# Kernel tuning notes

Measured on AMD Instinct MI355X. Metric: run time of the kernel, lower is better.

The kernel has to match this reference:

```python
import jax, jax.numpy as jnp
import numpy as np

N_NODES = 50000
N_EDGES = 800000
N_FEAT = 64
N_HID = 64
N_CLASSES = 10
N_GRAPHS = 64


def setup_inputs() -> dict:
    key = jax.random.key(0)
    ks = jax.random.split(key, 14)
    # edge_index with no self-loops (PyG add_remaining_self_loops then appends
    # exactly one self loop per node, which the reference reproduces)
    row = jax.random.randint(ks[0], (N_EDGES,), 0, N_NODES, dtype=jnp.int32)
    off = jax.random.randint(ks[1], (N_EDGES,), 1, N_NODES, dtype=jnp.int32)
    col = (row + off) % N_NODES
    edge_index = jnp.stack([row, col])
    batch = jnp.sort(jax.random.randint(ks[2], (N_NODES,), 0, N_GRAPHS, dtype=jnp.int32))
    x = jax.random.normal(ks[3], (N_NODES, N_FEAT), jnp.float32)
    P_vec = jax.random.normal(ks[4], (N_EDGES,), jnp.float32)

    def lin(k, fi, fo):
        return jax.random.normal(k, (fi, fo), jnp.float32) * (1.0 / np.sqrt(fi))

    return {
        "x": x, "edge_index": edge_index, "batch": batch, "P_vec": P_vec,
        "W1": lin(ks[5], N_FEAT, N_HID), "b1": jax.random.normal(ks[6], (N_HID,)) * 0.02,
        "W2": lin(ks[7], N_HID, N_HID), "b2": jax.random.normal(ks[8], (N_HID,)) * 0.02,
        "W3": lin(ks[9], N_HID, N_HID), "b3": jax.random.normal(ks[10], (N_HID,)) * 0.02,
        "Wl": lin(ks[11], N_HID, N_CLASSES), "bl": jax.random.normal(ks[12], (N_CLASSES,)) * 0.02,
    }


def reference(x, edge_index, batch, P_vec, W1, b1, W2, b2, W3, b3, Wl, bl):
    n = x.shape[0]
    row, col = edge_index[0], edge_index[1]
    # add_remaining_self_loops: append one self loop per node with weight 1.0
    sl = jnp.arange(n, dtype=row.dtype)
    fr = jnp.concatenate([row, sl])          # [E+N] source
    fc = jnp.concatenate([col, sl])          # [E+N] target (flow source_to_target)
    w = jnp.concatenate([jax.nn.sigmoid(P_vec), jnp.ones((n,), x.dtype)])
    deg = jax.ops.segment_sum(w, fc, num_segments=n)
    dis = jnp.where(deg > 0, deg ** -0.5, 0.0)  # deg_inv_sqrt, inf->0
    norm = dis[fr] * w * dis[fc]             # identical for all 3 conv layers

    def gcn_layer(h, W, b):
        h = h @ W                             # Linear (no bias inside lin)
        agg = jax.ops.segment_sum(norm[:, None] * h[fr], fc, num_segments=n)
        return agg + b

    h = jax.nn.relu(gcn_layer(x, W1, b1))
    h = jax.nn.relu(gcn_layer(h, W2, b2))
    h = gcn_layer(h, W3, b3)
    # global_mean_pool over batch segment ids
    sums = jax.ops.segment_sum(h, batch, num_segments=N_GRAPHS)
    cnt = jax.ops.segment_sum(jnp.ones((n, 1), h.dtype), batch, num_segments=N_GRAPHS)
    pooled = sums / jnp.maximum(cnt, 1.0)
    # dropout is identity at inference; final classifier
    return pooled @ Wl + bl
```

## Files before the change

### kernel.cpp

```cpp
#include <hip/hip_runtime.h>
#include <hip/hip_bf16.h>
#include <hip/hip_fp16.h>
#include <math.h>

#define N_GRAPHS 64
#define N_CLASSES 10
#define FIXSCALE 262144.0f
#define MAXDEG 64

typedef __hip_bfloat16 bf16;
typedef int          i32x4 __attribute__((ext_vector_type(4)));
typedef unsigned int u32x4 __attribute__((ext_vector_type(4)));
typedef _Float16     f16x8 __attribute__((ext_vector_type(8)));
typedef float        f32x4 __attribute__((ext_vector_type(4)));

__device__ __forceinline__ unsigned int pack_edge(int r, float s) {
    return ((unsigned int)r << 16) | (unsigned int)__half_as_ushort(__float2half(s));
}

__global__ void init_k(const float* __restrict__ P, const int* __restrict__ row,
                       unsigned int* __restrict__ packed, uint2* __restrict__ pre,
                       float* __restrict__ sums, float* __restrict__ cntG,
                       int n, int E) {
    int i = blockIdx.x * 256 + threadIdx.x;
    if (i < n) packed[i] = 0u;
    if (i < N_GRAPHS * 64) sums[i] = 0.0f;
    if (i < N_GRAPHS) cntG[i] = 0.0f;
    if (i < E) {
        float s = 1.0f / (1.0f + expf(-P[i]));
        pre[i] = make_uint2(pack_edge(row[i], s), (unsigned int)(s * FIXSCALE + 0.5f));
    }
}

__device__ __forceinline__ int bucket_of(int c) {
    int b = (int)(((unsigned int)c * 41u) >> 18);
    return b > 7 ? 7 : b;
}

__device__ __forceinline__ void do_edge(int c, unsigned int rec, unsigned int fix, int myb,
                                        unsigned int* __restrict__ packed,
                                        unsigned int* __restrict__ ell) {
    if (bucket_of(c) == myb) {
        unsigned int old = atomicAdd(&packed[c], (1u << 24) | fix);
        unsigned int rank = old >> 24;
        if (rank < MAXDEG) ell[c * MAXDEG + rank] = rec;
    }
}

__global__ __launch_bounds__(256) void hist_k(const uint2* __restrict__ pre,
                                              const int* __restrict__ col,
                                              unsigned int* __restrict__ packed,
                                              unsigned int* __restrict__ ell, int E) {
    const int myb = blockIdx.x & 7;
    const int slice = blockIdx.x >> 3;
    const int E4 = E >> 2;
    const i32x4* col4 = (const i32x4*)col;
    const u32x4* pre4 = (const u32x4*)pre;
#pragma unroll
    for (int k = 0; k < 4; ++k) {
        int i4 = slice * 1024 + k * 256 + (int)threadIdx.x;
        if (i4 < E4) {
            i32x4 c  = col4[i4];
            u32x4 pa = pre4[2 * i4];
            u32x4 pb = pre4[2 * i4 + 1];
            do_edge(c[0], pa[0], pa[1], myb, packed, ell);
            do_edge(c[1], pa[2], pa[3], myb, packed, ell);
            do_edge(c[2], pb[0], pb[1], myb, packed, ell);
            do_edge(c[3], pb[2], pb[3], myb, packed, ell);
        }
    }
    if (slice == 0) {
        for (int e = E4 * 4 + (int)threadIdx.x; e < E; e += 256) {
            uint2 p = pre[e];
            do_edge(col[e], p.x, p.y, myb, packed, ell);
        }
    }
}

__global__ void disxg_k(const unsigned int* __restrict__ packed,
                        const float* __restrict__ x,
                        float* __restrict__ dis, bf16* __restrict__ xg,
                        unsigned int* __restrict__ ell, int n) {
    int i = blockIdx.x * 256 + threadIdx.x;
    if (i < n * 64) {
        int node = i >> 6;
        int lane = i & 63;
        unsigned int pk = packed[node];
        float deg = 1.0f + (float)(pk & 0xFFFFFFu) * (1.0f / FIXSCALE);
        float dv = 1.0f / sqrtf(deg);
        xg[i] = __float2bfloat16(x[i] * dv);
        if (lane == 0) dis[node] = dv;
        int cnt = (int)(pk >> 24);
        if (cnt > MAXDEG) cnt = MAXDEG;
        int pad = ((cnt + 15) & ~15) - cnt;
        if (lane < pad) ell[node * MAXDEG + cnt + lane] = 0u;
    }
}

__global__ void fold_k(const float* __restrict__ W3, const float* __restrict__ b3,
                       const float* __restrict__ Wl, const float* __restrict__ bl,
                       const float* __restrict__ W1, const float* __restrict__ W2,
                       float* __restrict__ Wc, float* __restrict__ bc,
                       __half* __restrict__ W1h, __half* __restrict__ W2h) {
    int t = blockIdx.x * 256 + threadIdx.x;
    if (t < 64 * N_CLASSES) {
        int k = t / N_CLASSES, c = t % N_CLASSES;
        float acc = 0.0f;
        for (int m = 0; m < 64; ++m) acc += W3[k * 64 + m] * Wl[m * N_CLASSES + c];
        Wc[t] = acc;
    }
    if (t < N_CLASSES) {
        float acc = bl[t];
        for (int m = 0; m < 64; ++m) acc += b3[m] * Wl[m * N_CLASSES + t];
        bc[t] = acc;
    }
    if (t < 8192) {
        int u = t & 4095;
        int j = u & 7, lane = (u >> 3) & 63, k2 = (u >> 9) & 1, tt = u >> 10;
        int srow = k2 * 32 + (lane >> 4) * 8 + j;
        int scol = tt * 16 + (lane & 15);
        const float* W = (t < 4096) ? W1 : W2;
        __half* Wh = (t < 4096) ? W1h : W2h;
        Wh[u] = __float2half(W[srow * 64 + scol]);
    }
}

__device__ __forceinline__ float edge_term(unsigned int v, const bf16* g, int lane) {
    int r = (int)(v >> 16);
    float s = __half2float(__ushort_as_half((unsigned short)(v & 0xFFFFu)));
    return s * __bfloat162float(g[r * 64 + lane]);
}

template <int OUTF>
__global__ __launch_bounds__(256) void agg_k(const bf16* __restrict__ g,
                                             const unsigned int* __restrict__ ell,
                                             const unsigned int* __restrict__ packed,
                                             const float* __restrict__ dis,
                                             float* __restrict__ out,
                                             __half* __restrict__ outH, int n) {
    int tid = threadIdx.x;
    int node = __builtin_amdgcn_readfirstlane(blockIdx.x * 4 + (tid >> 6));
    if (node >= n) return;
    int lane = tid & 63;

    float d = dis[node];
    int cnt = (int)(packed[node] >> 24);
    if (cnt > MAXDEG) cnt = MAXDEG;
    int cnt16 = (cnt + 15) & ~15;
    float acc = __bfloat162float(g[node * 64 + lane]);
    const unsigned int* rowp = ell + node * MAXDEG;

    float a[16];
#pragma unroll
    for (int t = 0; t < 16; ++t) a[t] = 0.0f;
    for (int j = 0; j < cnt16; j += 16) {
        unsigned int v[16];
#pragma unroll
        for (int t = 0; t < 16; ++t) v[t] = rowp[j + t];
#pragma unroll
        for (int t = 0; t < 16; ++t) a[t] += edge_term(v[t], g, lane);
    }
#pragma unroll
    for (int off = 8; off >= 1; off >>= 1)
#pragma unroll
        for (int t = 0; t < off; ++t) a[t] += a[t + off];
    acc += a[0];
    acc *= d;

    if (OUTF == 1) outH[(size_t)node * 64 + lane] = __float2half(acc);
    else           out[(size_t)node * 64 + lane] = acc;
}

__global__ __launch_bounds__(256) void gemm_k(const __half* __restrict__ A,
                                              const __half* __restrict__ Wsw,
                                              const float* __restrict__ b,
                                              const float* __restrict__ dis,
                                              bf16* __restrict__ outg, int n) {
    int tid = threadIdx.x;
    int grp = blockIdx.x * 4 + (tid >> 6);
    int rbase = grp * 16;
    if (rbase >= n) return;
    int l = tid & 63, lr = l & 15, lh = l >> 4;

    const f16x8* Ap = (const f16x8*)(A + (size_t)(rbase + lr) * 64 + lh * 8);
    f16x8 a0 = Ap[0];
    f16x8 a1 = Ap[4];
    const f16x8* Wp = (const f16x8*)Wsw;

    float dv[4];
#pragma unroll
    for (int r = 0; r < 4; ++r) dv[r] = dis[rbase + lh * 4 + r];

#pragma unroll
    for (int t = 0; t < 4; ++t) {
        f32x4 acc = {0.0f, 0.0f, 0.0f, 0.0f};
        acc = __builtin_amdgcn_mfma_f32_16x16x32_f16(a0, Wp[(t * 2 + 0) * 64 + l], acc, 0, 0, 0);
        acc = __builtin_amdgcn_mfma_f32_16x16x32_f16(a1, Wp[(t * 2 + 1) * 64 + l], acc, 0, 0, 0);
        int col = t * 16 + lr;
        float bc_ = b[col];
#pragma unroll
        for (int r = 0; r < 4; ++r) {
            float v = fmaxf(acc[r] + bc_, 0.0f) * dv[r];
            outg[(size_t)(rbase + lh * 4 + r) * 64 + col] = __float2bfloat16(v);
        }
    }
}

__global__ __launch_bounds__(256) void poolpart_k(const float* __restrict__ h,
                                                  const int* __restrict__ batch,
                                                  float* __restrict__ sums,
                                                  float* __restrict__ cntG, int n) {
    int wave = threadIdx.x >> 6, lane = threadIdx.x & 63;
    int base = blockIdx.x * 128 + wave * 32;
    if (base >= n) return;
    int end = base + 32; if (end > n) end = n;
    int g = batch[base];
    float acc = 0.0f;
    int run = 0;
    for (int i = base; i < end; ++i) {
        int gi = batch[i];
        if (gi != g) {
            atomicAdd(&sums[g * 64 + lane], acc);
            if (lane == 0) atomicAdd(&cntG[g], (float)run);
            g = gi; acc = 0.0f; run = 0;
        }
        acc += h[i * 64 + lane];
        ++run;
    }
    atomicAdd(&sums[g * 64 + lane], acc);
    if (lane == 0) atomicAdd(&cntG[g], (float)run);
}

__global__ void classify_k(const float* __restrict__ sums, const float* __restrict__ cntG,
                           const float* __restrict__ Wc, const float* __restrict__ bc,
                           float* __restrict__ out) {
    __shared__ float pooled[64];
    int g = blockIdx.x;
    int t = threadIdx.x;
    float inv = 1.0f / fmaxf(cntG[g], 1.0f);
    pooled[t] = sums[g * 64 + t] * inv;
    __syncthreads();
    if (t < N_CLASSES) {
        float acc = bc[t];
        for (int k = 0; k < 64; ++k) acc += pooled[k] * Wc[k * N_CLASSES + t];
        out[g * N_CLASSES + t] = acc;
    }
}

extern "C" void kernel_launch(void* const* d_in, const int* in_sizes, int n_in,
                              void* d_out, int out_size, void* d_ws, size_t ws_size,
                              hipStream_t stream) {
    const float* x     = (const float*)d_in[0];
    const int*   eidx  = (const int*)d_in[1];
    const int*   batch = (const int*)d_in[2];
    const float* P     = (const float*)d_in[3];
    const float* W1 = (const float*)d_in[4];
    const float* b1 = (const float*)d_in[5];
    const float* W2 = (const float*)d_in[6];
    const float* b2 = (const float*)d_in[7];
    const float* W3 = (const float*)d_in[8];
    const float* b3 = (const float*)d_in[9];
    const float* Wl = (const float*)d_in[10];
    const float* bl = (const float*)d_in[11];
    float* out = (float*)d_out;

    const int N = in_sizes[2];
    const int E = in_sizes[3];
    const int* row = eidx;
    const int* col = eidx + E;

    char* p = (char*)d_ws;
    unsigned int* ell = (unsigned int*)p; p += (size_t)N * MAXDEG * 4;
    float* bufF     = (float*)p; p += (size_t)N * 64 * 4;
    bf16*  xg       = (bf16*)p;  p += (size_t)N * 64 * 2;
    bf16*  gA       = (bf16*)p;  p += (size_t)N * 64 * 2;
    __half* aH      = (__half*)p; p += (size_t)N * 64 * 2;
    unsigned int* packed = (unsigned int*)p; p += (size_t)N * 4;
    float* dis      = (float*)p; p += (size_t)N * 4;
    float* sums     = (float*)p; p += (size_t)N_GRAPHS * 64 * 4;
    float* cntG     = (float*)p; p += (size_t)N_GRAPHS * 4;
    float* Wc       = (float*)p; p += (size_t)64 * N_CLASSES * 4;
    __half* W1h     = (__half*)p; p += 4096 * 2;
    __half* W2h     = (__half*)p; p += 4096 * 2;
    float* bc       = (float*)p; p += (size_t)N_CLASSES * 4;
    bf16*  gB       = xg;
    uint2* pre      = (uint2*)bufF;

    dim3 blk(256);
    int edgeG = (E + 255) / 256;
    int bigG  = (N * 64 + 255) / 256;

    init_k<<<edgeG, blk, 0, stream>>>(P, row, packed, pre, sums, cntG, N, E);
    int nslice = ((E >> 2) + 1023) / 1024;
    hist_k<<<nslice * 8, blk, 0, stream>>>(pre, col, packed, ell, E);
    disxg_k<<<bigG, blk, 0, stream>>>(packed, x, dis, xg, ell, N);
    fold_k<<<32, blk, 0, stream>>>(W3, b3, Wl, bl, W1, W2, Wc, bc, W1h, W2h);

    int aggG  = (N + 3) / 4;
    int gemmG = (N / 16 + 3) / 4;

    agg_k<1><<<aggG, blk, 0, stream>>>(xg, ell, packed, dis, nullptr, aH, N);
    gemm_k<<<gemmG, blk, 0, stream>>>(aH, W1h, b1, dis, gA, N);
    agg_k<1><<<aggG, blk, 0, stream>>>(gA, ell, packed, dis, nullptr, aH, N);
    gemm_k<<<gemmG, blk, 0, stream>>>(aH, W2h, b2, dis, gB, N);
    agg_k<0><<<aggG, blk, 0, stream>>>(gB, ell, packed, dis, bufF, nullptr, N);

    int poolG = (N + 127) / 128;
    poolpart_k<<<poolG, blk, 0, stream>>>(bufF, batch, sums, cntG, N);
    classify_k<<<N_GRAPHS, dim3(64), 0, stream>>>(sums, cntG, Wc, bc, out);
}
```

Before: 228.3 us.

## Fold weight prep into init kernel, nontemporal hist loads, atomic-load gather in last agg

Merges the fold_k weight-folding kernel into init_k as 33 extra blocks, which drops one kernel launch. hist_k now reads col and the pre-packed edge records with nontemporal loads so these streaming reads pollute the cache less. The last aggregation layer gathers neighbour features through relaxed agent-scope atomic 16-bit loads, which likely changes the cache policy on that gather, and the edge accumulation uses explicit fmaf. The atomic-load path may add per-load overhead in the gather-heavy inner loop.

```diff
diff --git a/kernel.cpp b/kernel.cpp
--- a/kernel.cpp
+++ b/kernel.cpp
@@ -21,7 +21,12 @@
 __global__ void init_k(const float* __restrict__ P, const int* __restrict__ row,
                        unsigned int* __restrict__ packed, uint2* __restrict__ pre,
                        float* __restrict__ sums, float* __restrict__ cntG,
-                       int n, int E) {
+                       int n, int E, int edgeG,
+                       const float* __restrict__ W3, const float* __restrict__ b3,
+                       const float* __restrict__ Wl, const float* __restrict__ bl,
+                       const float* __restrict__ W1, const float* __restrict__ W2,
+                       float* __restrict__ Wc, float* __restrict__ bc,
+                       __half* __restrict__ W1h, __half* __restrict__ W2h) {
     int i = blockIdx.x * 256 + threadIdx.x;
     if (i < n) packed[i] = 0u;
     if (i < N_GRAPHS * 64) sums[i] = 0.0f;
@@ -29,6 +34,30 @@
     if (i < E) {
         float s = 1.0f / (1.0f + expf(-P[i]));
         pre[i] = make_uint2(pack_edge(row[i], s), (unsigned int)(s * FIXSCALE + 0.5f));
+    }
+    int fb = blockIdx.x - edgeG;
+    if (fb >= 0) {
+        int t = fb * 256 + threadIdx.x;
+        if (t < 64 * N_CLASSES) {
+            int k = t / N_CLASSES, c = t % N_CLASSES;
+            float acc = 0.0f;
+            for (int m = 0; m < 64; ++m) acc += W3[k * 64 + m] * Wl[m * N_CLASSES + c];
+            Wc[t] = acc;
+        }
+        if (t < N_CLASSES) {
+            float acc = bl[t];
+            for (int m = 0; m < 64; ++m) acc += b3[m] * Wl[m * N_CLASSES + t];
+            bc[t] = acc;
+        }
+        if (t < 8192) {
+            int u = t & 4095;
+            int j = u & 7, lane = (u >> 3) & 63, k2 = (u >> 9) & 1, tt = u >> 10;
+            int srow = k2 * 32 + (lane >> 4) * 8 + j;
+            int scol = tt * 16 + (lane & 15);
+            const float* W = (t < 4096) ? W1 : W2;
+            __half* Wh = (t < 4096) ? W1h : W2h;
+            Wh[u] = __float2half(W[srow * 64 + scol]);
+        }
     }
 }
 
@@ -60,9 +89,9 @@
     for (int k = 0; k < 4; ++k) {
         int i4 = slice * 1024 + k * 256 + (int)threadIdx.x;
         if (i4 < E4) {
-            i32x4 c  = col4[i4];
-            u32x4 pa = pre4[2 * i4];
-            u32x4 pb = pre4[2 * i4 + 1];
+            i32x4 c  = __builtin_nontemporal_load(col4 + i4);
+            u32x4 pa = __builtin_nontemporal_load(pre4 + 2 * i4);
+            u32x4 pb = __builtin_nontemporal_load(pre4 + 2 * i4 + 1);
             do_edge(c[0], pa[0], pa[1], myb, packed, ell);
             do_edge(c[1], pa[2], pa[3], myb, packed, ell);
             do_edge(c[2], pb[0], pb[1], myb, packed, ell);
@@ -97,41 +126,7 @@
     }
 }
 
-__global__ void fold_k(const float* __restrict__ W3, const float* __restrict__ b3,
-                       const float* __restrict__ Wl, const float* __restrict__ bl,
-                       const float* __restrict__ W1, const float* __restrict__ W2,
-                       float* __restrict__ Wc, float* __restrict__ bc,
-                       __half* __restrict__ W1h, __half* __restrict__ W2h) {
-    int t = blockIdx.x * 256 + threadIdx.x;
-    if (t < 64 * N_CLASSES) {
-        int k = t / N_CLASSES, c = t % N_CLASSES;
-        float acc = 0.0f;
-        for (int m = 0; m < 64; ++m) acc += W3[k * 64 + m] * Wl[m * N_CLASSES + c];
-        Wc[t] = acc;
-    }
-    if (t < N_CLASSES) {
-        float acc = bl[t];
-        for (int m = 0; m < 64; ++m) acc += b3[m] * Wl[m * N_CLASSES + t];
-        bc[t] = acc;
-    }
-    if (t < 8192) {
-        int u = t & 4095;
-        int j = u & 7, lane = (u >> 3) & 63, k2 = (u >> 9) & 1, tt = u >> 10;
-        int srow = k2 * 32 + (lane >> 4) * 8 + j;
-        int scol = tt * 16 + (lane & 15);
-        const float* W = (t < 4096) ? W1 : W2;
-        __half* Wh = (t < 4096) ? W1h : W2h;
-        Wh[u] = __float2half(W[srow * 64 + scol]);
-    }
-}
-
-__device__ __forceinline__ float edge_term(unsigned int v, const bf16* g, int lane) {
-    int r = (int)(v >> 16);
-    float s = __half2float(__ushort_as_half((unsigned short)(v & 0xFFFFu)));
-    return s * __bfloat162float(g[r * 64 + lane]);
-}
-
-template <int OUTF>
+template <int OUTF, int SCZ>
 __global__ __launch_bounds__(256) void agg_k(const bf16* __restrict__ g,
                                              const unsigned int* __restrict__ ell,
                                              const unsigned int* __restrict__ packed,
@@ -158,7 +153,20 @@
 #pragma unroll
         for (int t = 0; t < 16; ++t) v[t] = rowp[j + t];
 #pragma unroll
-        for (int t = 0; t < 16; ++t) a[t] += edge_term(v[t], g, lane);
+        for (int t = 0; t < 16; ++t) {
+            int r = (int)(v[t] >> 16);
+            float s = __half2float(__ushort_as_half((unsigned short)(v[t] & 0xFFFFu)));
+            float gv;
+            if (SCZ) {
+                unsigned short u = __hip_atomic_load(
+                    (const unsigned short*)(g + (size_t)r * 64 + lane),
+                    __ATOMIC_RELAXED, __HIP_MEMORY_SCOPE_AGENT);
+                gv = __uint_as_float((unsigned int)u << 16);
+            } else {
+                gv = __bfloat162float(g[(size_t)r * 64 + lane]);
+            }
+            a[t] = fmaf(s, gv, a[t]);
+        }
     }
 #pragma unroll
     for (int off = 8; off >= 1; off >>= 1)
@@ -290,20 +298,20 @@
     int edgeG = (E + 255) / 256;
     int bigG  = (N * 64 + 255) / 256;
 
-    init_k<<<edgeG, blk, 0, stream>>>(P, row, packed, pre, sums, cntG, N, E);
+    init_k<<<edgeG + 33, blk, 0, stream>>>(P, row, packed, pre, sums, cntG, N, E, edgeG,
+                                           W3, b3, Wl, bl, W1, W2, Wc, bc, W1h, W2h);
     int nslice = ((E >> 2) + 1023) / 1024;
     hist_k<<<nslice * 8, blk, 0, stream>>>(pre, col, packed, ell, E);
     disxg_k<<<bigG, blk, 0, stream>>>(packed, x, dis, xg, ell, N);
-    fold_k<<<32, blk, 0, stream>>>(W3, b3, Wl, bl, W1, W2, Wc, bc, W1h, W2h);
 
     int aggG  = (N + 3) / 4;
     int gemmG = (N / 16 + 3) / 4;
 
-    agg_k<1><<<aggG, blk, 0, stream>>>(xg, ell, packed, dis, nullptr, aH, N);
+    agg_k<1, 0><<<aggG, blk, 0, stream>>>(xg, ell, packed, dis, nullptr, aH, N);
     gemm_k<<<gemmG, blk, 0, stream>>>(aH, W1h, b1, dis, gA, N);
-    agg_k<1><<<aggG, blk, 0, stream>>>(gA, ell, packed, dis, nullptr, aH, N);
+    agg_k<1, 0><<<aggG, blk, 0, stream>>>(gA, ell, packed, dis, nullptr, aH, N);
     gemm_k<<<gemmG, blk, 0, stream>>>(aH, W2h, b2, dis, gB, N);
-    agg_k<0><<<aggG, blk, 0, stream>>>(gB, ell, packed, dis, bufF, nullptr, N);
+    agg_k<0, 1><<<aggG, blk, 0, stream>>>(gB, ell, packed, dis, bufF, nullptr, N);
 
     int poolG = (N + 127) / 128;
     poolpart_k<<<poolG, blk, 0, stream>>>(bufF, batch, sums, cntG, N);
```

New measurement: 238.8 us. 1.05x slower.
